# Kernel tuning notes

Measured on AMD Instinct MI355X. Metric: run time of the kernel, lower is better.

Reference implementation:

```python
import jax, jax.numpy as jnp
import numpy as np

E = 16          # num_local_experts
K = 4           # experts_per_token
H = 2048        # hidden_size
I = 2048        # intermediate_size
LIMIT = 7.0     # swiglu_limit
ALPHA = 1.702   # glu_alpha


def setup_inputs() -> dict:
    key = jax.random.key(0)
    ks = jax.random.split(key, 9)
    int8 = lambda k, shp: jax.random.randint(k, shp, -127, 128).astype(jnp.float32)
    return {
        "hidden_states": jax.random.normal(ks[0], (1024, H), dtype=jnp.float32),
        "router_logits": jax.random.normal(ks[1], (1024, E), dtype=jnp.float32),
        "gate_up_proj": int8(ks[2], (E, H, 2 * I)),                      # int8 values in f32
        "gate_up_proj_scale": jax.random.uniform(ks[3], (E, 2 * I), minval=0.5, maxval=1.5) * 0.002,
        "gate_up_proj_bias": jax.random.normal(ks[4], (E, 2 * I), dtype=jnp.float32) * 0.01,
        "gate_up_smooth_scale": jnp.ones((E, I), dtype=jnp.float32),
        "down_proj": int8(ks[5], (E, I, H)),
        "down_proj_scale": jax.random.uniform(ks[6], (E, H), minval=0.5, maxval=1.5) * 0.002,
        "down_proj_bias": jax.random.normal(ks[7], (E, H), dtype=jnp.float32) * 0.01,
    }


def _dyn_quant(x):
    # per-token symmetric int8 dynamic quant (npu_dynamic_quant)
    scale = jnp.maximum(jnp.max(jnp.abs(x), axis=-1, keepdims=True) / 127.0, 1e-8)
    q = jnp.clip(jnp.round(x / scale), -127.0, 127.0)
    return q, scale


def reference(hidden_states, router_logits, gate_up_proj, gate_up_proj_scale,
              gate_up_proj_bias, gate_up_smooth_scale, down_proj,
              down_proj_scale, down_proj_bias):
    T = hidden_states.shape[0]
    C = (2 * T * K) // E

    # --- gating (npu_moe_gating_top_k: softmax + top-k, then renormalize) ---
    probs = jax.nn.softmax(router_logits, axis=-1)
    topk_w, topk_i = jax.lax.top_k(probs, K)                 # [T,K]
    topk_w = topk_w / jnp.sum(topk_w, axis=-1, keepdims=True)

    # --- per-token dynamic quant ---
    x_q, x_scale = _dyn_quant(hidden_states)                 # [T,H], [T,1]

    # --- dispatch (npu_moe_init_routing_v2): token-major expansion, capacity buckets ---
    flat_e = topk_i.reshape(-1)                              # [T*K] expert id per row
    flat_w = topk_w.reshape(-1)                              # [T*K]
    src = jnp.arange(T * K) // K                             # [T*K] source token
    onehot = jax.nn.one_hot(flat_e, E, dtype=jnp.int32)      # [T*K,E]
    pos = jnp.sum(jnp.cumsum(onehot, axis=0) * onehot, axis=1) - 1  # position within expert
    valid = pos < C
    slot = flat_e * C + jnp.where(valid, pos, 0)             # unique for valid rows
    vf = valid.astype(x_q.dtype)[:, None]
    x_disp = jnp.zeros((E * C, H), x_q.dtype).at[slot].add(x_q[src] * vf)
    s_disp = jnp.zeros((E * C, 1), x_scale.dtype).at[slot].add(x_scale[src] * vf)
    x_disp = x_disp.reshape(E, C, H)
    s_disp = s_disp.reshape(E, C, 1)

    gu_i32 = jnp.einsum('ech,ehf->ecf', x_disp, gate_up_proj)          # [E,C,2I]
    y = gu_i32 * s_disp * gate_up_proj_scale[:, None, :] + gate_up_proj_bias[:, None, :]

    # --- gpt-oss swiglu (activate_left, clamp_limit, alpha=1.702, glu_bias=1.0) ---
    gate = jnp.minimum(y[..., :I], LIMIT)
    up = jnp.clip(y[..., I:], -LIMIT, LIMIT)
    act = gate * jax.nn.sigmoid(ALPHA * gate) * (up + 1.0)
    act = act * gate_up_smooth_scale[:, None, :]

    # --- requant + grouped GEMM 2 + dequant ---
    h_q, h_scale = _dyn_quant(act)                                     # [E,C,I], [E,C,1]
    z_i32 = jnp.einsum('eci,eih->ech', h_q, down_proj)                 # [E,C,H]
    z = z_i32 * h_scale * down_proj_scale[:, None, :] + down_proj_bias[:, None, :]

    # --- combine (npu_moe_finalize_routing): weighted scatter-add per source token ---
    gathered = z.reshape(E * C, H)[slot]                               # [T*K,H]
    out = jnp.zeros((T, H), z.dtype).at[src].add(flat_w[:, None] * vf * gathered)
    return out
```

## Files before the change

### kernel.cpp

```cpp
#include <hip/hip_runtime.h>
#include <stdint.h>
#include <stddef.h>

#define T_TOK 1024
#define NE    16
#define TOPK  4
#define HID   2048
#define INTER 2048
#define CAP   512
#define GLIMIT 7.0f
#define GALPHA 1.702f

#define BM  128
#define BK  32
#define LDP 40

typedef __attribute__((ext_vector_type(8))) _Float16 half8;
typedef __attribute__((ext_vector_type(4))) float     f32x4;

__global__ __launch_bounds__(256) void gating_kernel(
    const float* __restrict__ logits, int* __restrict__ topki, float* __restrict__ topkw)
{
    int t = blockIdx.x * 256 + threadIdx.x;
    if (t >= T_TOK) return;
    float l[NE];
#pragma unroll
    for (int e = 0; e < NE; e++) l[e] = logits[t * NE + e];
    unsigned used = 0;
    float val[TOPK]; int idx[TOPK];
#pragma unroll
    for (int k = 0; k < TOPK; k++) {
        float bv = -3.4e38f; int bi = 0;
#pragma unroll
        for (int e = 0; e < NE; e++) {
            bool ok = (((used >> e) & 1u) == 0u) && (l[e] > bv);
            bv = ok ? l[e] : bv;
            bi = ok ? e : bi;
        }
        used |= (1u << bi); idx[k] = bi; val[k] = bv;
    }
    float m = val[0];
    float s = 0.f, w[TOPK];
#pragma unroll
    for (int k = 0; k < TOPK; k++) { w[k] = expf(val[k] - m); s += w[k]; }
    float inv = 1.0f / s;
#pragma unroll
    for (int k = 0; k < TOPK; k++) { topki[t * TOPK + k] = idx[k]; topkw[t * TOPK + k] = w[k] * inv; }
}

__global__ __launch_bounds__(256) void quant_x_kernel(
    const float* __restrict__ x, _Float16* __restrict__ xq, float* __restrict__ xs)
{
    int t = blockIdx.x;
    const float* row = x + (size_t)t * HID;
    __shared__ float red[256];
    float amax = 0.f;
    for (int i = threadIdx.x; i < HID; i += 256) amax = fmaxf(amax, fabsf(row[i]));
    red[threadIdx.x] = amax; __syncthreads();
    for (int s = 128; s > 0; s >>= 1) {
        if (threadIdx.x < s) red[threadIdx.x] = fmaxf(red[threadIdx.x], red[threadIdx.x + s]);
        __syncthreads();
    }
    float scale = fmaxf(red[0] / 127.0f, 1e-8f);
    if (threadIdx.x == 0) xs[t] = scale;
    for (int i = threadIdx.x; i < HID; i += 256) {
        float q = rintf(row[i] / scale);
        q = fminf(fmaxf(q, -127.f), 127.f);
        xq[(size_t)t * HID + i] = (_Float16)q;
    }
}

__global__ __launch_bounds__(1024) void routing_kernel(
    const int* __restrict__ topki, const float* __restrict__ topkw,
    int* __restrict__ row_src, float* __restrict__ row_w, int* __restrict__ counts)
{
    int wv = threadIdx.x >> 6;
    int lane = threadIdx.x & 63;
    int base = 0;
    for (int r0 = 0; r0 < T_TOK * TOPK; r0 += 64) {
        int r = r0 + lane;
        int e = topki[r];
        unsigned long long mask = __ballot(e == wv);
        int pre = __popcll(mask & ((1ULL << lane) - 1ULL));
        if (e == wv) {
            int pos = base + pre;
            if (pos < CAP) {
                row_src[wv * CAP + pos] = r >> 2;
                row_w[wv * CAP + pos] = topkw[r];
            }
        }
        base += __popcll(mask);
    }
    if (lane == 0) counts[wv] = (base < CAP) ? base : CAP;
}

__global__ __launch_bounds__(256) void gemm1_kernel(
    const _Float16* __restrict__ xq, const float* __restrict__ xs,
    const int* __restrict__ row_src, const int* __restrict__ counts,
    const float* __restrict__ gup, const float* __restrict__ gus,
    const float* __restrict__ gub, const float* __restrict__ smo,
    float* __restrict__ act)
{
    int nt = blockIdx.x;
    int mt = blockIdx.y;
    int e  = blockIdx.z;
    int count = counts[e];
    int m0 = mt * BM;
    if (m0 >= count) return;

    __shared__ _Float16 sA[BM * LDP];
    __shared__ _Float16 sB[128 * LDP];

    int t = threadIdx.x;
    int lane = t & 63, w = t >> 6;
    int n16 = lane & 15, quad = lane >> 4;

    int aM = t >> 1, aHalf = t & 1;
    int agr = m0 + aM;
    const _Float16* aptr = nullptr;
    if (agr < count) aptr = xq + (size_t)row_src[e * CAP + agr] * HID;

    f32x4 acc[2][8];
#pragma unroll
    for (int i = 0; i < 2; i++)
#pragma unroll
        for (int j = 0; j < 8; j++) acc[i][j] = (f32x4)0.0f;

    const float* gbase = gup + (size_t)e * HID * (2 * INTER);

    for (int k0 = 0; k0 < HID; k0 += BK) {
        __syncthreads();
        {
            int4 v0, v1;
            v0.x = v0.y = v0.z = v0.w = 0; v1 = v0;
            if (aptr) {
                const int4* s4 = (const int4*)(aptr + k0 + aHalf * 16);
                v0 = s4[0]; v1 = s4[1];
            }
            int4* d4 = (int4*)&sA[aM * LDP + aHalf * 16];
            d4[0] = v0; d4[1] = v1;
        }
        {
            int n = t & 63;
            int kr = (t >> 6) * 8;
#pragma unroll
            for (int h = 0; h < 2; h++) {
                const float* src = gbase + (size_t)(k0 + kr) * (2 * INTER) + h * INTER + nt * 64 + n;
#pragma unroll
                for (int i = 0; i < 8; i++)
                    sB[(h * 64 + n) * LDP + kr + i] = (_Float16)src[(size_t)i * (2 * INTER)];
            }
        }
        __syncthreads();

        half8 af[2], bfr[8];
#pragma unroll
        for (int mf = 0; mf < 2; mf++)
            af[mf] = *(const half8*)&sA[(w * 32 + mf * 16 + n16) * LDP + quad * 8];
#pragma unroll
        for (int nf = 0; nf < 8; nf++)
            bfr[nf] = *(const half8*)&sB[(nf * 16 + n16) * LDP + quad * 8];
#pragma unroll
        for (int mf = 0; mf < 2; mf++)
#pragma unroll
            for (int nf = 0; nf < 8; nf++)
                acc[mf][nf] = __builtin_amdgcn_mfma_f32_16x16x32_f16(af[mf], bfr[nf], acc[mf][nf], 0, 0, 0);
    }

    const float* gsc = gus + (size_t)e * (2 * INTER);
    const float* gbi = gub + (size_t)e * (2 * INTER);
    const float* sms = smo + (size_t)e * INTER;
#pragma unroll
    for (int mf = 0; mf < 2; mf++) {
#pragma unroll
        for (int r = 0; r < 4; r++) {
            int gr = m0 + w * 32 + mf * 16 + quad * 4 + r;
            if (gr >= count) continue;
            float srow = xs[row_src[e * CAP + gr]];
            float* arow = act + (size_t)(e * CAP + gr) * INTER;
#pragma unroll
            for (int g = 0; g < 4; g++) {
                int col = nt * 64 + g * 16 + n16;
                float yg = acc[mf][g][r]     * srow * gsc[col]         + gbi[col];
                float yu = acc[mf][g + 4][r] * srow * gsc[INTER + col] + gbi[INTER + col];
                float gate = fminf(yg, GLIMIT);
                float up   = fminf(fmaxf(yu, -GLIMIT), GLIMIT);
                float sig  = 1.0f / (1.0f + expf(-GALPHA * gate));
                arow[col] = gate * sig * (up + 1.0f) * sms[col];
            }
        }
    }
}

__global__ __launch_bounds__(256) void requant_kernel(
    const float* __restrict__ act, const int* __restrict__ counts,
    _Float16* __restrict__ hq, float* __restrict__ hs)
{
    int b = blockIdx.x;
    int e = b >> 9, c = b & (CAP - 1);
    if (c >= counts[e]) return;
    const float* row = act + (size_t)b * INTER;
    __shared__ float red[256];
    float amax = 0.f;
    for (int i = threadIdx.x; i < INTER; i += 256) amax = fmaxf(amax, fabsf(row[i]));
    red[threadIdx.x] = amax; __syncthreads();
    for (int s = 128; s > 0; s >>= 1) {
        if (threadIdx.x < s) red[threadIdx.x] = fmaxf(red[threadIdx.x], red[threadIdx.x + s]);
        __syncthreads();
    }
    float scale = fmaxf(red[0] / 127.0f, 1e-8f);
    if (threadIdx.x == 0) hs[b] = scale;
    for (int i = threadIdx.x; i < INTER; i += 256) {
        float q = rintf(row[i] / scale);
        q = fminf(fmaxf(q, -127.f), 127.f);
        hq[(size_t)b * INTER + i] = (_Float16)q;
    }
}

__global__ __launch_bounds__(256) void gemm2_kernel(
    const _Float16* __restrict__ hq, const float* __restrict__ hs,
    const int* __restrict__ row_src, const float* __restrict__ row_w,
    const int* __restrict__ counts, const float* __restrict__ dwn,
    const float* __restrict__ dsc, const float* __restrict__ dbi,
    float* __restrict__ out)
{
    int nt = blockIdx.x;
    int mt = blockIdx.y;
    int e  = blockIdx.z;
    int count = counts[e];
    int m0 = mt * BM;
    if (m0 >= count) return;

    __shared__ _Float16 sA[BM * LDP];
    __shared__ _Float16 sB[128 * LDP];

    int t = threadIdx.x;
    int lane = t & 63, w = t >> 6;
    int n16 = lane & 15, quad = lane >> 4;

    int aM = t >> 1, aHalf = t & 1;
    int agr = m0 + aM;
    const _Float16* aptr = nullptr;
    if (agr < count) aptr = hq + (size_t)(e * CAP + agr) * INTER;

    f32x4 acc[2][8];
#pragma unroll
    for (int i = 0; i < 2; i++)
#pragma unroll
        for (int j = 0; j < 8; j++) acc[i][j] = (f32x4)0.0f;

    const float* bbase = dwn + (size_t)e * INTER * HID;

    for (int k0 = 0; k0 < INTER; k0 += BK) {
        __syncthreads();
        {
            int4 v0, v1;
            v0.x = v0.y = v0.z = v0.w = 0; v1 = v0;
            if (aptr) {
                const int4* s4 = (const int4*)(aptr + k0 + aHalf * 16);
                v0 = s4[0]; v1 = s4[1];
            }
            int4* d4 = (int4*)&sA[aM * LDP + aHalf * 16];
            d4[0] = v0; d4[1] = v1;
        }
        {
            int n = t & 127;
            int kr = (t >> 7) * 16;
            const float* src = bbase + (size_t)(k0 + kr) * HID + nt * 128 + n;
#pragma unroll
            for (int i = 0; i < 16; i++)
                sB[n * LDP + kr + i] = (_Float16)src[(size_t)i * HID];
        }
        __syncthreads();

        half8 af[2], bfr[8];
#pragma unroll
        for (int mf = 0; mf < 2; mf++)
            af[mf] = *(const half8*)&sA[(w * 32 + mf * 16 + n16) * LDP + quad * 8];
#pragma unroll
        for (int nf = 0; nf < 8; nf++)
            bfr[nf] = *(const half8*)&sB[(nf * 16 + n16) * LDP + quad * 8];
#pragma unroll
        for (int mf = 0; mf < 2; mf++)
#pragma unroll
            for (int nf = 0; nf < 8; nf++)
                acc[mf][nf] = __builtin_amdgcn_mfma_f32_16x16x32_f16(af[mf], bfr[nf], acc[mf][nf], 0, 0, 0);
    }

    const float* dscE = dsc + (size_t)e * HID;
    const float* dbiE = dbi + (size_t)e * HID;
#pragma unroll
    for (int mf = 0; mf < 2; mf++) {
#pragma unroll
        for (int r = 0; r < 4; r++) {
            int gr = m0 + w * 32 + mf * 16 + quad * 4 + r;
            if (gr >= count) continue;
            int ri = e * CAP + gr;
            float hsr = hs[ri];
            float wr  = row_w[ri];
            float* orow = out + (size_t)row_src[ri] * HID;
#pragma unroll
            for (int nf = 0; nf < 8; nf++) {
                int col = nt * 128 + nf * 16 + n16;
                float z = acc[mf][nf][r] * hsr * dscE[col] + dbiE[col];
                atomicAdd(&orow[col], wr * z);
            }
        }
    }
}

extern "C" void kernel_launch(void* const* d_in, const int* in_sizes, int n_in,
                              void* d_out, int out_size, void* d_ws, size_t ws_size,
                              hipStream_t stream)
{
    (void)in_sizes; (void)n_in; (void)out_size; (void)ws_size;
    const float* x   = (const float*)d_in[0];
    const float* rl  = (const float*)d_in[1];
    const float* gup = (const float*)d_in[2];
    const float* gus = (const float*)d_in[3];
    const float* gub = (const float*)d_in[4];
    const float* smo = (const float*)d_in[5];
    const float* dwn = (const float*)d_in[6];
    const float* dsc = (const float*)d_in[7];
    const float* dbi = (const float*)d_in[8];
    float* out = (float*)d_out;

    char* p = (char*)d_ws;
    auto carve = [&](size_t bytes) -> char* {
        char* r = p; p += (bytes + 255) & ~(size_t)255; return r;
    };
    _Float16* xq   = (_Float16*)carve((size_t)T_TOK * HID * 2);
    float* xs      = (float*)carve((size_t)T_TOK * 4);
    int* topki     = (int*)carve((size_t)T_TOK * TOPK * 4);
    float* topkw   = (float*)carve((size_t)T_TOK * TOPK * 4);
    int* counts    = (int*)carve((size_t)NE * 4);
    int* rsrc      = (int*)carve((size_t)NE * CAP * 4);
    float* rw      = (float*)carve((size_t)NE * CAP * 4);
    float* actb    = (float*)carve((size_t)NE * CAP * INTER * 4);
    _Float16* hq   = (_Float16*)carve((size_t)NE * CAP * INTER * 2);
    float* hsb     = (float*)carve((size_t)NE * CAP * 4);

    hipMemsetAsync(d_out, 0, (size_t)T_TOK * HID * 4, stream);
    gating_kernel<<<dim3((T_TOK + 255) / 256), 256, 0, stream>>>(rl, topki, topkw);
    quant_x_kernel<<<dim3(T_TOK), 256, 0, stream>>>(x, xq, xs);
    routing_kernel<<<dim3(1), 1024, 0, stream>>>(topki, topkw, rsrc, rw, counts);
    gemm1_kernel<<<dim3(INTER / 64, CAP / BM, NE), 256, 0, stream>>>(
        xq, xs, rsrc, counts, gup, gus, gub, smo, actb);
    requant_kernel<<<dim3(NE * CAP), 256, 0, stream>>>(actb, counts, hq, hsb);
    gemm2_kernel<<<dim3(HID / 128, CAP / BM, NE), 256, 0, stream>>>(
        hq, hsb, rsrc, rw, counts, dwn, dsc, dbi, out);
}
```

Measured before the change: 1.078 ms.

## Pre-transpose weights to fp16, use direct global-to-LDS loads and swizzled tiles

Adds a per-call kernel that converts and transposes the f32 expert weights into K-contiguous fp16 buffers, so both GEMMs can stage tiles with 16-byte global_load_lds into XOR-swizzled LDS using BK=64 and a 4x4 MFMA tile per wave. The intermediate activation is stored as fp16 instead of f32, and the quant/requant kernels are vectorized to 8 elements per thread. The aim is to remove the strided scalar f32 weight loads and per-element conversion in the GEMM inner loops. In exchange it adds an extra full pass that reads all weights and writes fp16 copies every call, plus workspace for them.

Result: slower. 1.250 ms (+15.9%).

```diff
diff --git a/kernel.cpp b/kernel.cpp
--- a/kernel.cpp
+++ b/kernel.cpp
@@ -10,13 +10,16 @@
 #define CAP   512
 #define GLIMIT 7.0f
 #define GALPHA 1.702f
-
-#define BM  128
-#define BK  32
-#define LDP 40
+#define BKH   64
 
 typedef __attribute__((ext_vector_type(8))) _Float16 half8;
 typedef __attribute__((ext_vector_type(4))) float     f32x4;
+
+__device__ inline void gld16(const void* g, void* l) {
+    __builtin_amdgcn_global_load_lds(
+        (const __attribute__((address_space(1))) unsigned int*)g,
+        (__attribute__((address_space(3))) unsigned int*)l, 16, 0, 0);
+}
 
 __global__ __launch_bounds__(256) void gating_kernel(
     const float* __restrict__ logits, int* __restrict__ topki, float* __restrict__ topkw)
@@ -54,8 +57,10 @@
     int t = blockIdx.x;
     const float* row = x + (size_t)t * HID;
     __shared__ float red[256];
-    float amax = 0.f;
-    for (int i = threadIdx.x; i < HID; i += 256) amax = fmaxf(amax, fabsf(row[i]));
+    float4 v0 = *(const float4*)(row + threadIdx.x * 8);
+    float4 v1 = *(const float4*)(row + threadIdx.x * 8 + 4);
+    float amax = fmaxf(fmaxf(fmaxf(fabsf(v0.x), fabsf(v0.y)), fmaxf(fabsf(v0.z), fabsf(v0.w))),
+                       fmaxf(fmaxf(fabsf(v1.x), fabsf(v1.y)), fmaxf(fabsf(v1.z), fabsf(v1.w))));
     red[threadIdx.x] = amax; __syncthreads();
     for (int s = 128; s > 0; s >>= 1) {
         if (threadIdx.x < s) red[threadIdx.x] = fmaxf(red[threadIdx.x], red[threadIdx.x + s]);
@@ -63,11 +68,15 @@
     }
     float scale = fmaxf(red[0] / 127.0f, 1e-8f);
     if (threadIdx.x == 0) xs[t] = scale;
-    for (int i = threadIdx.x; i < HID; i += 256) {
-        float q = rintf(row[i] / scale);
-        q = fminf(fmaxf(q, -127.f), 127.f);
-        xq[(size_t)t * HID + i] = (_Float16)q;
-    }
+    float inv = 1.0f / scale;
+    float q[8] = {v0.x, v0.y, v0.z, v0.w, v1.x, v1.y, v1.z, v1.w};
+    half8 o;
+#pragma unroll
+    for (int i = 0; i < 8; i++) {
+        float qq = fminf(fmaxf(rintf(q[i] * inv), -127.f), 127.f);
+        o[i] = (_Float16)qq;
+    }
+    *(half8*)(xq + (size_t)t * HID + threadIdx.x * 8) = o;
 }
 
 __global__ __launch_bounds__(1024) void routing_kernel(
@@ -94,115 +103,162 @@
     if (lane == 0) counts[wv] = (base < CAP) ? base : CAP;
 }
 
+__global__ __launch_bounds__(256) void wtrans_kernel(
+    const float* __restrict__ W, _Float16* __restrict__ Wt, int N, int K)
+{
+    int e = blockIdx.z;
+    const float* We = W + (size_t)e * K * N;
+    _Float16* Wte = Wt + (size_t)e * N * K;
+    int n0 = blockIdx.x * 64, k0 = blockIdx.y * 64;
+    __shared__ _Float16 sT[64][72];
+    int t = threadIdx.x;
+    int kr = t >> 2;
+    int nb = (t & 3) * 16;
+    const float* src = We + (size_t)(k0 + kr) * N + n0 + nb;
+#pragma unroll
+    for (int i = 0; i < 4; i++) {
+        float4 v = *(const float4*)(src + i * 4);
+        sT[nb + i * 4 + 0][kr] = (_Float16)v.x;
+        sT[nb + i * 4 + 1][kr] = (_Float16)v.y;
+        sT[nb + i * 4 + 2][kr] = (_Float16)v.z;
+        sT[nb + i * 4 + 3][kr] = (_Float16)v.w;
+    }
+    __syncthreads();
+    int nr = t >> 2, seg = t & 3;
+    _Float16* dst = Wte + (size_t)(n0 + nr) * K + k0 + seg * 16;
+    int4 a = *(const int4*)&sT[nr][seg * 16];
+    int4 b = *(const int4*)&sT[nr][seg * 16 + 8];
+    *(int4*)dst = a;
+    *(int4*)(dst + 8) = b;
+}
+
 __global__ __launch_bounds__(256) void gemm1_kernel(
     const _Float16* __restrict__ xq, const float* __restrict__ xs,
     const int* __restrict__ row_src, const int* __restrict__ counts,
-    const float* __restrict__ gup, const float* __restrict__ gus,
-    const float* __restrict__ gub, const float* __restrict__ smo,
-    float* __restrict__ act)
+    const _Float16* __restrict__ wt1,
+    const float* __restrict__ gus, const float* __restrict__ gub,
+    const float* __restrict__ smo, _Float16* __restrict__ act)
 {
     int nt = blockIdx.x;
     int mt = blockIdx.y;
     int e  = blockIdx.z;
     int count = counts[e];
-    int m0 = mt * BM;
+    int m0 = mt * 128;
     if (m0 >= count) return;
 
-    __shared__ _Float16 sA[BM * LDP];
-    __shared__ _Float16 sB[128 * LDP];
+    __shared__ _Float16 sA[128 * BKH];
+    __shared__ _Float16 sB[128 * BKH];
 
     int t = threadIdx.x;
-    int lane = t & 63, w = t >> 6;
+    int wv = t >> 6, lane = t & 63;
     int n16 = lane & 15, quad = lane >> 4;
-
-    int aM = t >> 1, aHalf = t & 1;
-    int agr = m0 + aM;
-    const _Float16* aptr = nullptr;
-    if (agr < count) aptr = xq + (size_t)row_src[e * CAP + agr] * HID;
-
-    f32x4 acc[2][8];
-#pragma unroll
-    for (int i = 0; i < 2; i++)
-#pragma unroll
-        for (int j = 0; j < 8; j++) acc[i][j] = (f32x4)0.0f;
-
-    const float* gbase = gup + (size_t)e * HID * (2 * INTER);
-
-    for (int k0 = 0; k0 < HID; k0 += BK) {
-        __syncthreads();
-        {
-            int4 v0, v1;
-            v0.x = v0.y = v0.z = v0.w = 0; v1 = v0;
-            if (aptr) {
-                const int4* s4 = (const int4*)(aptr + k0 + aHalf * 16);
-                v0 = s4[0]; v1 = s4[1];
-            }
-            int4* d4 = (int4*)&sA[aM * LDP + aHalf * 16];
-            d4[0] = v0; d4[1] = v1;
-        }
-        {
-            int n = t & 63;
-            int kr = (t >> 6) * 8;
-#pragma unroll
-            for (int h = 0; h < 2; h++) {
-                const float* src = gbase + (size_t)(k0 + kr) * (2 * INTER) + h * INTER + nt * 64 + n;
-#pragma unroll
-                for (int i = 0; i < 8; i++)
-                    sB[(h * 64 + n) * LDP + kr + i] = (_Float16)src[(size_t)i * (2 * INTER)];
-            }
-        }
-        __syncthreads();
-
-        half8 af[2], bfr[8];
-#pragma unroll
-        for (int mf = 0; mf < 2; mf++)
-            af[mf] = *(const half8*)&sA[(w * 32 + mf * 16 + n16) * LDP + quad * 8];
-#pragma unroll
-        for (int nf = 0; nf < 8; nf++)
-            bfr[nf] = *(const half8*)&sB[(nf * 16 + n16) * LDP + quad * 8];
-#pragma unroll
-        for (int mf = 0; mf < 2; mf++)
-#pragma unroll
-            for (int nf = 0; nf < 8; nf++)
-                acc[mf][nf] = __builtin_amdgcn_mfma_f32_16x16x32_f16(af[mf], bfr[nf], acc[mf][nf], 0, 0, 0);
+    int seg = lane & 7, rsub = lane >> 3;
+    int swz8 = (seg ^ rsub) * 8;
+
+    const _Float16* wte = wt1 + (size_t)e * 4096 * 2048;
+    const _Float16* aSrc[4];
+    const _Float16* bSrc[4];
+    _Float16* aDst[4];
+    _Float16* bDst[4];
+#pragma unroll
+    for (int j = 0; j < 4; j++) {
+        int rr = wv * 32 + j * 8 + rsub;
+        int gr = m0 + rr;
+        int cl = gr < count ? gr : (count - 1);
+        aSrc[j] = xq + (size_t)row_src[e * CAP + cl] * HID + swz8;
+        int nIdx = (rr < 64) ? (nt * 64 + rr) : (2048 + nt * 64 + (rr - 64));
+        bSrc[j] = wte + (size_t)nIdx * 2048 + swz8;
+        aDst[j] = &sA[(wv * 32 + j * 8) * BKH];
+        bDst[j] = &sB[(wv * 32 + j * 8) * BKH];
+    }
+
+    int rhalf = (wv & 1) * 64, chalf = (wv >> 1) * 32;
+    int aOff[4][2], bOff[4][2];
+#pragma unroll
+    for (int mf = 0; mf < 4; mf++)
+#pragma unroll
+        for (int ks = 0; ks < 2; ks++) {
+            int row = rhalf + mf * 16 + n16;
+            aOff[mf][ks] = row * BKH + (((ks * 4 + quad) ^ (row & 7)) * 8);
+        }
+#pragma unroll
+    for (int nf = 0; nf < 4; nf++)
+#pragma unroll
+        for (int ks = 0; ks < 2; ks++) {
+            int row = (nf < 2) ? (chalf + nf * 16 + n16) : (64 + chalf + (nf - 2) * 16 + n16);
+            bOff[nf][ks] = row * BKH + (((ks * 4 + quad) ^ (row & 7)) * 8);
+        }
+
+    f32x4 acc[4][4];
+#pragma unroll
+    for (int i = 0; i < 4; i++)
+#pragma unroll
+        for (int j = 0; j < 4; j++) acc[i][j] = (f32x4)0.0f;
+
+    for (int k0 = 0; k0 < HID; k0 += BKH) {
+        __syncthreads();
+#pragma unroll
+        for (int j = 0; j < 4; j++) {
+            gld16(aSrc[j], aDst[j]);
+            gld16(bSrc[j], bDst[j]);
+            aSrc[j] += BKH; bSrc[j] += BKH;
+        }
+        __syncthreads();
+#pragma unroll
+        for (int ks = 0; ks < 2; ks++) {
+            half8 af[4], bf[4];
+#pragma unroll
+            for (int mf = 0; mf < 4; mf++) af[mf] = *(const half8*)&sA[aOff[mf][ks]];
+#pragma unroll
+            for (int nf = 0; nf < 4; nf++) bf[nf] = *(const half8*)&sB[bOff[nf][ks]];
+#pragma unroll
+            for (int mf = 0; mf < 4; mf++)
+#pragma unroll
+                for (int nf = 0; nf < 4; nf++)
+                    acc[mf][nf] = __builtin_amdgcn_mfma_f32_16x16x32_f16(af[mf], bf[nf], acc[mf][nf], 0, 0, 0);
+        }
     }
 
     const float* gsc = gus + (size_t)e * (2 * INTER);
     const float* gbi = gub + (size_t)e * (2 * INTER);
     const float* sms = smo + (size_t)e * INTER;
-#pragma unroll
-    for (int mf = 0; mf < 2; mf++) {
+    int cg = nt * 64 + chalf;
+#pragma unroll
+    for (int mf = 0; mf < 4; mf++) {
 #pragma unroll
         for (int r = 0; r < 4; r++) {
-            int gr = m0 + w * 32 + mf * 16 + quad * 4 + r;
+            int gr = m0 + rhalf + mf * 16 + quad * 4 + r;
             if (gr >= count) continue;
             float srow = xs[row_src[e * CAP + gr]];
-            float* arow = act + (size_t)(e * CAP + gr) * INTER;
-#pragma unroll
-            for (int g = 0; g < 4; g++) {
-                int col = nt * 64 + g * 16 + n16;
-                float yg = acc[mf][g][r]     * srow * gsc[col]         + gbi[col];
-                float yu = acc[mf][g + 4][r] * srow * gsc[INTER + col] + gbi[INTER + col];
+            _Float16* arow = act + (size_t)(e * CAP + gr) * INTER;
+#pragma unroll
+            for (int nf = 0; nf < 2; nf++) {
+                int col = cg + nf * 16 + n16;
+                float yg = acc[mf][nf][r]     * srow * gsc[col]         + gbi[col];
+                float yu = acc[mf][nf + 2][r] * srow * gsc[INTER + col] + gbi[INTER + col];
                 float gate = fminf(yg, GLIMIT);
                 float up   = fminf(fmaxf(yu, -GLIMIT), GLIMIT);
                 float sig  = 1.0f / (1.0f + expf(-GALPHA * gate));
-                arow[col] = gate * sig * (up + 1.0f) * sms[col];
+                arow[col] = (_Float16)(gate * sig * (up + 1.0f) * sms[col]);
             }
         }
     }
 }
 
 __global__ __launch_bounds__(256) void requant_kernel(
-    const float* __restrict__ act, const int* __restrict__ counts,
+    const _Float16* __restrict__ act, const int* __restrict__ counts,
     _Float16* __restrict__ hq, float* __restrict__ hs)
 {
     int b = blockIdx.x;
     int e = b >> 9, c = b & (CAP - 1);
     if (c >= counts[e]) return;
-    const float* row = act + (size_t)b * INTER;
+    const _Float16* row = act + (size_t)b * INTER;
     __shared__ float red[256];
+    half8 v = *(const half8*)(row + threadIdx.x * 8);
+    float f[8];
     float amax = 0.f;
-    for (int i = threadIdx.x; i < INTER; i += 256) amax = fmaxf(amax, fabsf(row[i]));
+#pragma unroll
+    for (int i = 0; i < 8; i++) { f[i] = (float)v[i]; amax = fmaxf(amax, fabsf(f[i])); }
     red[threadIdx.x] = amax; __syncthreads();
     for (int s = 128; s > 0; s >>= 1) {
         if (threadIdx.x < s) red[threadIdx.x] = fmaxf(red[threadIdx.x], red[threadIdx.x + s]);
@@ -210,17 +266,21 @@
     }
     float scale = fmaxf(red[0] / 127.0f, 1e-8f);
     if (threadIdx.x == 0) hs[b] = scale;
-    for (int i = threadIdx.x; i < INTER; i += 256) {
-        float q = rintf(row[i] / scale);
-        q = fminf(fmaxf(q, -127.f), 127.f);
-        hq[(size_t)b * INTER + i] = (_Float16)q;
-    }
+    float inv = 1.0f / scale;
+    half8 o;
+#pragma unroll
+    for (int i = 0; i < 8; i++) {
+        float q = fminf(fmaxf(rintf(f[i] * inv), -127.f), 127.f);
+        o[i] = (_Float16)q;
+    }
+    *(half8*)(hq + (size_t)b * INTER + threadIdx.x * 8) = o;
 }
 
 __global__ __launch_bounds__(256) void gemm2_kernel(
     const _Float16* __restrict__ hq, const float* __restrict__ hs,
     const int* __restrict__ row_src, const float* __restrict__ row_w,
-    const int* __restrict__ counts, const float* __restrict__ dwn,
+    const int* __restrict__ counts,
+    const _Float16* __restrict__ wt2,
     const float* __restrict__ dsc, const float* __restrict__ dbi,
     float* __restrict__ out)
 {
@@ -228,80 +288,96 @@
     int mt = blockIdx.y;
     int e  = blockIdx.z;
     int count = counts[e];
-    int m0 = mt * BM;
+    int m0 = mt * 128;
     if (m0 >= count) return;
 
-    __shared__ _Float16 sA[BM * LDP];
-    __shared__ _Float16 sB[128 * LDP];
+    __shared__ _Float16 sA[128 * BKH];
+    __shared__ _Float16 sB[128 * BKH];
 
     int t = threadIdx.x;
-    int lane = t & 63, w = t >> 6;
+    int wv = t >> 6, lane = t & 63;
     int n16 = lane & 15, quad = lane >> 4;
-
-    int aM = t >> 1, aHalf = t & 1;
-    int agr = m0 + aM;
-    const _Float16* aptr = nullptr;
-    if (agr < count) aptr = hq + (size_t)(e * CAP + agr) * INTER;
-
-    f32x4 acc[2][8];
-#pragma unroll
-    for (int i = 0; i < 2; i++)
-#pragma unroll
-        for (int j = 0; j < 8; j++) acc[i][j] = (f32x4)0.0f;
-
-    const float* bbase = dwn + (size_t)e * INTER * HID;
-
-    for (int k0 = 0; k0 < INTER; k0 += BK) {
-        __syncthreads();
-        {
-            int4 v0, v1;
-            v0.x = v0.y = v0.z = v0.w = 0; v1 = v0;
-            if (aptr) {
-                const int4* s4 = (const int4*)(aptr + k0 + aHalf * 16);
-                v0 = s4[0]; v1 = s4[1];
-            }
-            int4* d4 = (int4*)&sA[aM * LDP + aHalf * 16];
-            d4[0] = v0; d4[1] = v1;
-        }
-        {
-            int n = t & 127;
-            int kr = (t >> 7) * 16;
-            const float* src = bbase + (size_t)(k0 + kr) * HID + nt * 128 + n;
-#pragma unroll
-            for (int i = 0; i < 16; i++)
-                sB[n * LDP + kr + i] = (_Float16)src[(size_t)i * HID];
-        }
-        __syncthreads();
-
-        half8 af[2], bfr[8];
-#pragma unroll
-        for (int mf = 0; mf < 2; mf++)
-            af[mf] = *(const half8*)&sA[(w * 32 + mf * 16 + n16) * LDP + quad * 8];
-#pragma unroll
-        for (int nf = 0; nf < 8; nf++)
-            bfr[nf] = *(const half8*)&sB[(nf * 16 + n16) * LDP + quad * 8];
-#pragma unroll
-        for (int mf = 0; mf < 2; mf++)
-#pragma unroll
-            for (int nf = 0; nf < 8; nf++)
-                acc[mf][nf] = __builtin_amdgcn_mfma_f32_16x16x32_f16(af[mf], bfr[nf], acc[mf][nf], 0, 0, 0);
+    int seg = lane & 7, rsub = lane >> 3;
+    int swz8 = (seg ^ rsub) * 8;
+
+    const _Float16* wte = wt2 + (size_t)e * 2048 * 2048;
+    const _Float16* aSrc[4];
+    const _Float16* bSrc[4];
+    _Float16* aDst[4];
+    _Float16* bDst[4];
+#pragma unroll
+    for (int j = 0; j < 4; j++) {
+        int rr = wv * 32 + j * 8 + rsub;
+        int gr = m0 + rr;
+        int cl = gr < count ? gr : (count - 1);
+        aSrc[j] = hq + (size_t)(e * CAP + cl) * INTER + swz8;
+        bSrc[j] = wte + (size_t)(nt * 128 + rr) * 2048 + swz8;
+        aDst[j] = &sA[(wv * 32 + j * 8) * BKH];
+        bDst[j] = &sB[(wv * 32 + j * 8) * BKH];
+    }
+
+    int rhalf = (wv & 1) * 64, chalf = (wv >> 1) * 64;
+    int aOff[4][2], bOff[4][2];
+#pragma unroll
+    for (int mf = 0; mf < 4; mf++)
+#pragma unroll
+        for (int ks = 0; ks < 2; ks++) {
+            int row = rhalf + mf * 16 + n16;
+            aOff[mf][ks] = row * BKH + (((ks * 4 + quad) ^ (row & 7)) * 8);
+        }
+#pragma unroll
+    for (int nf = 0; nf < 4; nf++)
+#pragma unroll
+        for (int ks = 0; ks < 2; ks++) {
+            int row = chalf + nf * 16 + n16;
+            bOff[nf][ks] = row * BKH + (((ks * 4 + quad) ^ (row & 7)) * 8);
+        }
+
+    f32x4 acc[4][4];
+#pragma unroll
+    for (int i = 0; i < 4; i++)
+#pragma unroll
+        for (int j = 0; j < 4; j++) acc[i][j] = (f32x4)0.0f;
+
+    for (int k0 = 0; k0 < INTER; k0 += BKH) {
+        __syncthreads();
+#pragma unroll
+        for (int j = 0; j < 4; j++) {
+            gld16(aSrc[j], aDst[j]);
+            gld16(bSrc[j], bDst[j]);
+            aSrc[j] += BKH; bSrc[j] += BKH;
+        }
+        __syncthreads();
+#pragma unroll
+        for (int ks = 0; ks < 2; ks++) {
+            half8 af[4], bf[4];
+#pragma unroll
+            for (int mf = 0; mf < 4; mf++) af[mf] = *(const half8*)&sA[aOff[mf][ks]];
+#pragma unroll
+            for (int nf = 0; nf < 4; nf++) bf[nf] = *(const half8*)&sB[bOff[nf][ks]];
+#pragma unroll
+            for (int mf = 0; mf < 4; mf++)
+#pragma unroll
+                for (int nf = 0; nf < 4; nf++)
+                    acc[mf][nf] = __builtin_amdgcn_mfma_f32_16x16x32_f16(af[mf], bf[nf], acc[mf][nf], 0, 0, 0);
+        }
     }
 
     const float* dscE = dsc + (size_t)e * HID;
     const float* dbiE = dbi + (size_t)e * HID;
 #pragma unroll
-    for (int mf = 0; mf < 2; mf++) {
+    for (int mf = 0; mf < 4; mf++) {
 #pragma unroll
         for (int r = 0; r < 4; r++) {
-            int gr = m0 + w * 32 + mf * 16 + quad * 4 + r;
+            int gr = m0 + rhalf + mf * 16 + quad * 4 + r;
             if (gr >= count) continue;
             int ri = e * CAP + gr;
             float hsr = hs[ri];
             float wr  = row_w[ri];
             float* orow = out + (size_t)row_src[ri] * HID;
 #pragma unroll
-            for (int nf = 0; nf < 8; nf++) {
-                int col = nt * 128 + nf * 16 + n16;
+            for (int nf = 0; nf < 4; nf++) {
+                int col = nt * 128 + chalf + nf * 16 + n16;
                 float z = acc[mf][nf][r] * hsr * dscE[col] + dbiE[col];
                 atomicAdd(&orow[col], wr * z);
             }
@@ -336,7 +412,9 @@
     int* counts    = (int*)carve((size_t)NE * 4);
     int* rsrc      = (int*)carve((size_t)NE * CAP * 4);
     float* rw      = (float*)carve((size_t)NE * CAP * 4);
-    float* actb    = (float*)carve((size_t)NE * CAP * INTER * 4);
+    _Float16* wt1  = (_Float16*)carve((size_t)NE * 4096 * 2048 * 2);
+    _Float16* wt2  = (_Float16*)carve((size_t)NE * 2048 * 2048 * 2);
+    _Float16* actb = (_Float16*)carve((size_t)NE * CAP * INTER * 2);
     _Float16* hq   = (_Float16*)carve((size_t)NE * CAP * INTER * 2);
     float* hsb     = (float*)carve((size_t)NE * CAP * 4);
 
@@ -344,9 +422,11 @@
     gating_kernel<<<dim3((T_TOK + 255) / 256), 256, 0, stream>>>(rl, topki, topkw);
     quant_x_kernel<<<dim3(T_TOK), 256, 0, stream>>>(x, xq, xs);
     routing_kernel<<<dim3(1), 1024, 0, stream>>>(topki, topkw, rsrc, rw, counts);
-    gemm1_kernel<<<dim3(INTER / 64, CAP / BM, NE), 256, 0, stream>>>(
-        xq, xs, rsrc, counts, gup, gus, gub, smo, actb);
+    wtrans_kernel<<<dim3(64, 32, NE), 256, 0, stream>>>(gup, wt1, 2 * INTER, HID);
+    wtrans_kernel<<<dim3(32, 32, NE), 256, 0, stream>>>(dwn, wt2, HID, INTER);
+    gemm1_kernel<<<dim3(32, 4, NE), 256, 0, stream>>>(
+        xq, xs, rsrc, counts, wt1, gus, gub, smo, actb);
     requant_kernel<<<dim3(NE * CAP), 256, 0, stream>>>(actb, counts, hq, hsb);
-    gemm2_kernel<<<dim3(HID / 128, CAP / BM, NE), 256, 0, stream>>>(
-        hq, hsb, rsrc, rw, counts, dwn, dsc, dbi, out);
-}
+    gemm2_kernel<<<dim3(16, 4, NE), 256, 0, stream>>>(
+        hq, hsb, rsrc, rw, counts, wt2, dsc, dbi, out);
+}
```
